# Kernel tuning notes

Measured on AMD Instinct MI355X. Metric: run time of the kernel, lower is better.

Reference implementation:

```python
import jax, jax.numpy as jnp
import numpy as np

N, E, ESM, H, OUT, L, NG = 20000, 640000, 1280, 128, 256, 3, 64
NV, EV = 4, 1  # node/edge vector channels
MSG_S, MSG_V = 2 * H + H, 2 * NV + EV   # 384, 9
UPD_S, UPD_V = 2 * H, 2 * NV            # 256, 8


def _safe_norm(v):
    # exact ||v|| with zero (not nan) gradient at v == 0
    n2 = jnp.sum(v * v, axis=-1)
    pos = n2 > 0
    return jnp.sqrt(jnp.where(pos, n2, 1.0)) * pos


def _normalize(x, eps=1e-12):
    n = _safe_norm(x)[..., None]
    return jnp.where(n > 0, x / jnp.maximum(n, eps), 0.0)


def _ln(x, g, b, eps=1e-5):
    m = x.mean(-1, keepdims=True)
    v = ((x - m) ** 2).mean(-1, keepdims=True)
    return (x - m) / jnp.sqrt(v + eps) * g + b


def _gvp(s, v, Wss, Wvs, Wsv, Wvv, g, b):
    # s: [M, Cs], v: [M, Cv, 3]
    vn = _safe_norm(v)                                        # [M, Cv]
    s_out = jax.nn.gelu(_ln(s @ Wss.T + vn @ Wvs.T, g, b), approximate=False)
    v_out = jnp.einsum('mic,oi->moc', v, Wvv)                 # [M, Cvo, 3]
    v_out = v_out * jax.nn.sigmoid(s @ Wsv.T)[:, :, None]     # gate from input s
    return s_out, v_out


def _compute_node_vectors(coords, cb):
    ca_cb = _normalize(cb - coords)
    ca_next = jnp.roll(coords, -1, axis=0)
    d = (ca_next - coords).at[-1].set(0.0)
    d = _normalize(d)
    normal = _normalize(jnp.cross(ca_cb, d))
    t = (ca_next - jnp.roll(coords, 1, axis=0)).at[0].set(0.0).at[-1].set(0.0)
    t = _normalize(t)
    return jnp.stack([ca_cb, d, normal, t], axis=1)           # [N, 4, 3]


def setup_inputs() -> dict:
    key = jax.random.key(0)
    ks = jax.random.split(key, 32)

    def w(k, shape):
        return (jax.random.normal(k, shape, jnp.float32) / np.sqrt(shape[-1])).astype(jnp.float32)

    inp = {
        'esm_features': jax.random.normal(ks[0], (N, ESM), jnp.float32),
        'geometric_features': jax.random.normal(ks[1], (N, 15), jnp.float32),
        'node_coords': jax.random.normal(ks[2], (N, 3), jnp.float32) * 10.0,
        'edge_index': jax.random.randint(ks[3], (2, E), 0, N, jnp.int32),
        'edge_attr': jax.random.normal(ks[4], (E, 16), jnp.float32),
        'batch_index': jnp.sort(jax.random.randint(ks[5], (N,), 0, NG, jnp.int32)),
        # projections
        'node_proj_W': w(ks[6], (H, ESM + 9)), 'node_proj_b': jnp.zeros((H,), jnp.float32),
        'edge_proj_W': w(ks[7], (H, 13)), 'edge_proj_b': jnp.zeros((H,), jnp.float32),
        # message GVP (stacked over L layers)
        'msg_Wss': w(ks[8], (L, H, MSG_S)), 'msg_Wvs': w(ks[9], (L, H, MSG_V)),
        'msg_Wsv': w(ks[10], (L, NV, MSG_S)), 'msg_Wvv': w(ks[11], (L, NV, MSG_V)),
        'msg_ln_g': jnp.ones((L, H), jnp.float32), 'msg_ln_b': jnp.zeros((L, H), jnp.float32),
        # update GVP
        'upd_Wss': w(ks[12], (L, H, UPD_S)), 'upd_Wvs': w(ks[13], (L, H, UPD_V)),
        'upd_Wsv': w(ks[14], (L, NV, UPD_S)), 'upd_Wvv': w(ks[15], (L, NV, UPD_V)),
        'upd_ln_g': jnp.ones((L, H), jnp.float32), 'upd_ln_b': jnp.zeros((L, H), jnp.float32),
        # heads
        'node_out_W': w(ks[16], (ESM, H)), 'node_out_b': jnp.zeros((ESM,), jnp.float32),
        'graph_out_W': w(ks[17], (OUT, H)), 'graph_out_b': jnp.zeros((OUT,), jnp.float32),
    }
    return inp


def reference(esm_features, geometric_features, node_coords, edge_index, edge_attr,
              batch_index, node_proj_W, node_proj_b, edge_proj_W, edge_proj_b,
              msg_Wss, msg_Wvs, msg_Wsv, msg_Wvv, msg_ln_g, msg_ln_b,
              upd_Wss, upd_Wvs, upd_Wsv, upd_Wvv, upd_ln_g, upd_ln_b,
              node_out_W, node_out_b, graph_out_W, graph_out_b):
    n = esm_features.shape[0]
    cb = geometric_features[:, 3:6]
    geo_scalar = geometric_features[:, 6:15]
    node_s = jnp.concatenate([esm_features, geo_scalar], -1) @ node_proj_W.T + node_proj_b
    node_v = _compute_node_vectors(node_coords, cb)
    edge_s = jnp.concatenate([edge_attr[:, 0:2], edge_attr[:, 5:]], -1) @ edge_proj_W.T + edge_proj_b
    edge_v = edge_attr[:, 2:5][:, None, :]                    # [E, 1, 3]
    src, dst = edge_index[0], edge_index[1]
    for l in range(msg_Wss.shape[0]):
        ms = jnp.concatenate([node_s[src], node_s[dst], edge_s], -1)   # [E, 3H]
        mv = jnp.concatenate([node_v[src], node_v[dst], edge_v], 1)    # [E, 9, 3]
        ms, mv = _gvp(ms, mv, msg_Wss[l], msg_Wvs[l], msg_Wsv[l], msg_Wvv[l],
                      msg_ln_g[l], msg_ln_b[l])
        ag_s = jnp.zeros((n, ms.shape[1]), ms.dtype).at[dst].add(ms)
        ag_v = jnp.zeros((n, mv.shape[1], 3), mv.dtype).at[dst].add(mv)
        us = jnp.concatenate([node_s, ag_s], -1)
        uv = jnp.concatenate([node_v, ag_v], 1)
        ns, nv = _gvp(us, uv, upd_Wss[l], upd_Wvs[l], upd_Wsv[l], upd_Wvv[l],
                      upd_ln_g[l], upd_ln_b[l])
        node_s = node_s + ns
        node_v = node_v + nv
    updated_nodes = node_s @ node_out_W.T + node_out_b
    gfeat = node_s @ graph_out_W.T + graph_out_b
    cnt = jax.ops.segment_sum(jnp.ones((n,), gfeat.dtype), batch_index, NG)
    graph_emb = jax.ops.segment_sum(gfeat, batch_index, NG) / jnp.maximum(cnt, 1.0)[:, None]
    return graph_emb, updated_nodes
```

## Files before the change

### kernel.cpp

```cpp
#include <hip/hip_runtime.h>
#include <math.h>

#define DEVI __device__ __forceinline__

namespace {

constexpr int NN = 20000;
constexpr int NE = 640000;

DEVI float gelu_f(float x){ return 0.5f*x*(1.0f+erff(x*0.70710678118654752440f)); }
DEVI float gelu_t(float x){
  float u = x*x;
  float z = x*(1.59576912f + 0.07135481f*u);
  return x / (1.f + __expf(-z));
}
DEVI float sigm(float x){ return 1.0f/(1.0f+expf(-x)); }
DEVI float sigm_f(float x){ return 1.0f/(1.0f+__expf(-x)); }

struct F3{ float x,y,z; };
DEVI F3 sub3(F3 a, F3 b){ return F3{a.x-b.x, a.y-b.y, a.z-b.z}; }
DEVI F3 cross3(F3 a, F3 b){ return F3{a.y*b.z-a.z*b.y, a.z*b.x-a.x*b.z, a.x*b.y-a.y*b.x}; }
DEVI F3 snorm3(F3 v){
  float n2 = v.x*v.x+v.y*v.y+v.z*v.z;
  if(n2 > 0.f){ float inv = 1.0f/sqrtf(n2); return F3{v.x*inv, v.y*inv, v.z*inv}; }
  return F3{0.f,0.f,0.f};
}

__global__ void k_tr(const float* __restrict__ src, float* __restrict__ dst,
                     int R, int C, int ld, int coff){
  int idx = blockIdx.x*256 + threadIdx.x;
  if(idx >= R*C) return;
  int r = idx / C, c = idx % C;
  dst[c*R + r] = src[r*ld + coff + c];
}

__global__ __launch_bounds__(256,4) void k_init(
                       const float* __restrict__ esm, const float* __restrict__ geo,
                       const float* __restrict__ Wt, const float* __restrict__ bias,
                       float* __restrict__ node_s){
  __shared__ float s_l[16][64];
  int t = threadIdx.x;
  int o = t&127, h = t>>7;
  int n0 = blockIdx.x*16;
  float acc[8];
#pragma unroll
  for(int i=0;i<8;i++) acc[i]=0.f;
  for(int k0=0;k0<1289;k0+=64){
    int kmax = (1289-k0 < 64) ? (1289-k0) : 64;
    for(int idx=t; idx<1024; idx+=256){
      int n = idx>>6, k = idx&63;
      float v = 0.f;
      int kk = k0+k;
      if(k < kmax){
        v = (kk<1280) ? esm[(size_t)(n0+n)*1280 + kk] : geo[(n0+n)*15 + 6 + (kk-1280)];
      }
      s_l[n][k] = v;
    }
    __syncthreads();
    int kq = kmax & ~3;
    for(int k=0;k<kq;k+=4){
      float w0 = Wt[(k0+k)*128+o];
      float w1 = Wt[(k0+k+1)*128+o];
      float w2 = Wt[(k0+k+2)*128+o];
      float w3 = Wt[(k0+k+3)*128+o];
#pragma unroll
      for(int n=0;n<8;n++){
        float4 s4 = *reinterpret_cast<const float4*>(&s_l[h*8+n][k]);
        acc[n] += s4.x*w0 + s4.y*w1 + s4.z*w2 + s4.w*w3;
      }
    }
    for(int k=kq;k<kmax;k++){
      float w = Wt[(k0+k)*128+o];
#pragma unroll
      for(int n=0;n<8;n++) acc[n] += s_l[h*8+n][k]*w;
    }
    __syncthreads();
  }
  float b = bias[o];
#pragma unroll
  for(int n=0;n<8;n++) node_s[(size_t)(n0+h*8+n)*128 + o] = acc[n] + b;
}

__global__ void k_nodevec(const float* __restrict__ coords, const float* __restrict__ geo,
                          float* __restrict__ node_v){
  int n = blockIdx.x*256 + threadIdx.x;
  if(n>=NN) return;
  F3 c  {coords[n*3], coords[n*3+1], coords[n*3+2]};
  F3 cb {geo[n*15+3], geo[n*15+4], geo[n*15+5]};
  F3 cacb = snorm3(sub3(cb, c));
  F3 d{0.f,0.f,0.f};
  if(n < NN-1){
    F3 nx {coords[(n+1)*3], coords[(n+1)*3+1], coords[(n+1)*3+2]};
    d = snorm3(sub3(nx, c));
  }
  F3 nor = snorm3(cross3(cacb, d));
  F3 tv{0.f,0.f,0.f};
  if(n>0 && n<NN-1){
    F3 nx {coords[(n+1)*3], coords[(n+1)*3+1], coords[(n+1)*3+2]};
    F3 pv {coords[(n-1)*3], coords[(n-1)*3+1], coords[(n-1)*3+2]};
    tv = snorm3(sub3(nx, pv));
  }
  float* p = node_v + n*12;
  p[0]=cacb.x; p[1]=cacb.y; p[2]=cacb.z;
  p[3]=d.x;    p[4]=d.y;    p[5]=d.z;
  p[6]=nor.x;  p[7]=nor.y;  p[8]=nor.z;
  p[9]=tv.x;   p[10]=tv.y;  p[11]=tv.z;
}

__global__ void k_hist(const int* __restrict__ eidx, int* __restrict__ counts){
  int e = blockIdx.x*256+threadIdx.x;
  if(e>=NE) return;
  atomicAdd(&counts[eidx[NE+e]], 1);
}
__global__ void k_cntg(const int* __restrict__ batch, int* __restrict__ cntg){
  int n = blockIdx.x*256+threadIdx.x;
  if(n>=NN) return;
  atomicAdd(&cntg[batch[n]], 1);
}
__global__ void k_scan1(const int* __restrict__ counts, int* __restrict__ bsums){
  __shared__ int red[256];
  int b=blockIdx.x, t=threadIdx.x;
  int base=b*512;
  int v=0;
  for(int i=t;i<512;i+=256){ int g=base+i; if(g<NN) v+=counts[g]; }
  red[t]=v; __syncthreads();
  for(int s=128;s;s>>=1){ if(t<s) red[t]+=red[t+s]; __syncthreads(); }
  if(t==0) bsums[b]=red[0];
}
__global__ void k_scan2(int* bsums){
  if(threadIdx.x==0 && blockIdx.x==0){
    int run=0;
    for(int i=0;i<40;i++){ int v=bsums[i]; bsums[i]=run; run+=v; }
  }
}
__global__ void k_scan3(const int* __restrict__ counts, const int* __restrict__ bsums,
                        int* __restrict__ offs){
  __shared__ int c_l[512];
  int b=blockIdx.x, t=threadIdx.x, base=b*512;
  for(int i=t;i<512;i+=256){ int g=base+i; c_l[i] = (g<NN)? counts[g]:0; }
  __syncthreads();
  if(t==0){
    int run=bsums[b];
    for(int i=0;i<512;i++){
      int g=base+i;
      if(g<NN) offs[g]=run;
      run += c_l[i];
    }
    if(b==39) offs[NN]=run;
  }
}
__global__ void k_fill(const int* __restrict__ eidx, int* __restrict__ cursor,
                       const float* __restrict__ eattr,
                       int* __restrict__ srcp, float* __restrict__ ea_s){
  int e = blockIdx.x*256+threadIdx.x;
  if(e>=NE) return;
  int d = eidx[NE+e];
  int s = eidx[e];
  int pos = atomicAdd(&cursor[d], 1);
  srcp[pos] = s;
  const float4* src4 = reinterpret_cast<const float4*>(eattr + (size_t)e*16);
  float4* dst4 = reinterpret_cast<float4*>(ea_s + (size_t)pos*16);
  dst4[0]=src4[0]; dst4[1]=src4[1]; dst4[2]=src4[2]; dst4[3]=src4[3];
}

__global__ __launch_bounds__(256,4) void k_pre(
                      const float* __restrict__ node_s, const float* __restrict__ node_v,
                      const float* __restrict__ Wt_ss, const float* __restrict__ Wt_vs,
                      const float* __restrict__ Wsv, const float* __restrict__ Wvv,
                      float* __restrict__ P_a, float* __restrict__ P_b,
                      float* __restrict__ G_a, float* __restrict__ G_b,
                      float* __restrict__ V_a, float* __restrict__ V_b){
  __shared__ float s_l[16][128];
  __shared__ float nv_l[16][4];
  __shared__ float uv[16][12];
  int t = threadIdx.x;
  int n0 = blockIdx.x*16;
  for(int idx=t; idx<2048; idx+=256){
    int n = idx>>7, k = idx&127;
    s_l[n][k] = node_s[(size_t)(n0+n)*128 + k];
  }
  if(t<192){ int n=t/12, k=t%12; uv[n][k] = node_v[(n0+n)*12+k]; }
  __syncthreads();
  if(t<64){
    int n=t>>2, j=t&3;
    float x=uv[n][j*3], y=uv[n][j*3+1], z=uv[n][j*3+2];
    float n2=x*x+y*y+z*z;
    nv_l[n][j] = n2>0.f ? sqrtf(n2) : 0.f;
  }
  if(t<192){
    int n=t/12, k=t%12, c=k/3, x=k-c*3;
    float va=0.f, vb=0.f;
#pragma unroll
    for(int j=0;j<4;j++){
      float vv = uv[n][j*3+x];
      va += Wvv[c*9+j]*vv;
      vb += Wvv[c*9+4+j]*vv;
    }
    V_a[(n0+n)*12+k]=va; V_b[(n0+n)*12+k]=vb;
  }
  if(t<128){
    int n=t>>3, c=(t>>1)&3, hh=t&1;
    const float* w = Wsv + c*384 + hh*128;
    float g=0.f;
    for(int k=0;k<128;k++) g += s_l[n][k]*w[k];
    (hh ? G_b : G_a)[(n0+n)*4+c] = g;
  }
  __syncthreads();
  int o = t&127, h = t>>7;
  float acc[16];
#pragma unroll
  for(int i=0;i<16;i++) acc[i]=0.f;
  const float* Wb = Wt_ss + h*128*128;
  for(int k=0;k<128;k++){
    float w = Wb[k*128+o];
#pragma unroll
    for(int n=0;n<16;n++) acc[n] += s_l[n][k]*w;
  }
  const float* Wv = Wt_vs + h*4*128;
#pragma unroll
  for(int j=0;j<4;j++){
    float w = Wv[j*128+o];
#pragma unroll
    for(int n=0;n<16;n++) acc[n] += nv_l[n][j]*w;
  }
  float* P = h ? P_b : P_a;
#pragma unroll
  for(int n=0;n<16;n++) P[(size_t)(n0+n)*128+o] = acc[n];
}

__global__ void k_econst(const float* __restrict__ Wss, const float* __restrict__ Wvs,
                         const float* __restrict__ Wsv, const float* __restrict__ Wvv,
                         const float* __restrict__ Wep, const float* __restrict__ epb,
                         float* __restrict__ ec){
  int t=threadIdx.x;
  for(int idx=t; idx<13*128; idx+=256){
    int j=idx>>7, o=idx&127;
    float s=0.f;
    for(int k=0;k<128;k++) s += Wss[o*384+256+k]*Wep[k*13+j];
    ec[j*128+o]=s;
  }
  for(int o=t;o<128;o+=256){
    float s=0.f;
    for(int k=0;k<128;k++) s += Wss[o*384+256+k]*epb[k];
    ec[1664+o]=s;
    ec[1792+o]=Wvs[o*9+8];
  }
  if(t<52){ int c=t/13,j=t%13; float s=0.f; for(int k=0;k<128;k++) s+=Wsv[c*384+256+k]*Wep[k*13+j]; ec[1920+t]=s; }
  if(t<4){ float s=0.f; for(int k=0;k<128;k++) s+=Wsv[t*384+256+k]*epb[k]; ec[1972+t]=s; ec[1976+t]=Wvv[t*9+8]; }
}

#define DECLST(P) int P##s=0; float4 P##A0{},P##A1{},P##A2{},P##A3{}; \
                  float P##pax=0.f,P##pay=0.f,P##ga=0.f,P##va=0.f;
#define LOADST(P, IDX) do{ int _p=(IDX); \
  P##s = srcp[_p]; \
  const float4* _ea = reinterpret_cast<const float4*>(ea_s + (size_t)_p*16); \
  P##A0=_ea[0]; P##A1=_ea[1]; P##A2=_ea[2]; P##A3=_ea[3]; \
  const float* _pa = P_a + (size_t)P##s*128; \
  P##pax=_pa[lane]; P##pay=_pa[64+lane]; \
  if(lane<12){ P##ga=G_a[(size_t)P##s*4+cv]; P##va=V_a[(size_t)P##s*12+lane]; } \
}while(0)
#define COMPUTE(P) do{ \
  float e0=P##A0.x,e1=P##A0.y,e2=P##A1.y,e3=P##A1.z,e4=P##A1.w, \
        e5=P##A2.x,e6=P##A2.y,e7=P##A2.z,e8=P##A2.w,e9=P##A3.x, \
        e10=P##A3.y,e11=P##A3.z,e12=P##A3.w; \
  float evx=P##A0.z, evy=P##A0.w, evz=P##A1.x; \
  float en2 = evx*evx+evy*evy+evz*evz; \
  float evn = en2>0.f ? sqrtf(en2) : 0.f; \
  float px = fmaf(evn,W8x, P##pax + Bx); \
  float py = fmaf(evn,W8y, P##pay + By); \
  px=fmaf(me2x[0],e0,px);   py=fmaf(me2y[0],e0,py); \
  px=fmaf(me2x[1],e1,px);   py=fmaf(me2y[1],e1,py); \
  px=fmaf(me2x[2],e2,px);   py=fmaf(me2y[2],e2,py); \
  px=fmaf(me2x[3],e3,px);   py=fmaf(me2y[3],e3,py); \
  px=fmaf(me2x[4],e4,px);   py=fmaf(me2y[4],e4,py); \
  px=fmaf(me2x[5],e5,px);   py=fmaf(me2y[5],e5,py); \
  px=fmaf(me2x[6],e6,px);   py=fmaf(me2y[6],e6,py); \
  px=fmaf(me2x[7],e7,px);   py=fmaf(me2y[7],e7,py); \
  px=fmaf(me2x[8],e8,px);   py=fmaf(me2y[8],e8,py); \
  px=fmaf(me2x[9],e9,px);   py=fmaf(me2y[9],e9,py); \
  px=fmaf(me2x[10],e10,px); py=fmaf(me2y[10],e10,py); \
  px=fmaf(me2x[11],e11,px); py=fmaf(me2y[11],e11,py); \
  px=fmaf(me2x[12],e12,px); py=fmaf(me2y[12],e12,py); \
  float sm = px+py; \
  float sq = px*px + py*py; \
  _Pragma("unroll") \
  for(int m=32;m;m>>=1){ sm += __shfl_xor(sm,m); sq += __shfl_xor(sq,m); } \
  float mean = sm*0.0078125f; \
  float var  = fmaf(sq,0.0078125f, -mean*mean); \
  float rstd = rsqrtf((var>0.f?var:0.f) + 1e-5f); \
  accx += gelu_t(fmaf((px-mean)*rstd, LGx, LBx)); \
  accy += gelu_t(fmaf((py-mean)*rstd, LGy, LBy)); \
  if(lane<12){ \
    const float* gcl = s_gcol + cv*13; \
    float g = P##ga + gbc; \
    g=fmaf(gcl[0],e0,g); g=fmaf(gcl[1],e1,g); g=fmaf(gcl[2],e2,g); \
    g=fmaf(gcl[3],e3,g); g=fmaf(gcl[4],e4,g); g=fmaf(gcl[5],e5,g); \
    g=fmaf(gcl[6],e6,g); g=fmaf(gcl[7],e7,g); g=fmaf(gcl[8],e8,g); \
    g=fmaf(gcl[9],e9,g); g=fmaf(gcl[10],e10,g); g=fmaf(gcl[11],e11,g); \
    g=fmaf(gcl[12],e12,g); \
    float gt = sigm_f(g); \
    float evc = (xv==0) ? evx : ((xv==1) ? evy : evz); \
    avk = fmaf(fmaf(wvc,evc, P##va + vbk), gt, avk); \
  } \
}while(0)

__global__ __launch_bounds__(256,4) void k_msg(
                      const float* __restrict__ P_a, const float* __restrict__ P_b,
                      const float* __restrict__ G_a, const float* __restrict__ G_b,
                      const float* __restrict__ V_a, const float* __restrict__ V_b,
                      const float* __restrict__ ea_s, const int* __restrict__ srcp,
                      const int* __restrict__ offs,
                      const float* __restrict__ ec,
                      const float* __restrict__ lng, const float* __restrict__ lnb,
                      float* __restrict__ ag_s, float* __restrict__ ag_v){
  __shared__ float s_gcol[52];
  int t = threadIdx.x;
  if(t<52) s_gcol[t]=ec[1920+t];
  int n = blockIdx.x*4 + (t>>6);
  int lane = t&63;
  float me2x[13], me2y[13];
#pragma unroll
  for(int j=0;j<13;j++){ me2x[j]=ec[j*128+lane]; me2y[j]=ec[j*128+64+lane]; }
  float Bx = ec[1664+lane]    + P_b[(size_t)n*128+lane];
  float By = ec[1664+64+lane] + P_b[(size_t)n*128+64+lane];
  float W8x = ec[1792+lane], W8y = ec[1792+64+lane];
  float LGx = lng[lane], LGy = lng[64+lane];
  float LBx = lnb[lane], LBy = lnb[64+lane];
  int cv = lane/3, xv = lane - cv*3;
  float vbk=0.f, gbc=0.f, wvc=0.f;
  if(lane<12){
    vbk = V_b[(size_t)n*12+lane];
    gbc = G_b[(size_t)n*4+cv] + ec[1972+cv];
    wvc = ec[1976+cv];
  }
  __syncthreads();
  float accx=0.f, accy=0.f, avk=0.f;
  int beg = offs[n], end = offs[n+1];
  DECLST(a_) DECLST(b_)
  int idx = beg;
  if(beg < end) LOADST(a_, beg);
  while(idx + 1 < end){
    LOADST(b_, idx+1);
    COMPUTE(a_);
    if(idx + 2 < end) LOADST(a_, idx+2);
    COMPUTE(b_);
    idx += 2;
  }
  if(idx < end) COMPUTE(a_);
  ag_s[(size_t)n*128+lane]    = accx;
  ag_s[(size_t)n*128+64+lane] = accy;
  if(lane<12) ag_v[(size_t)n*12+lane] = avk;
}

__global__ __launch_bounds__(256,4) void k_update(
                         float* __restrict__ node_s, float* __restrict__ node_v,
                         const float* __restrict__ ag_s, const float* __restrict__ ag_v,
                         const float* __restrict__ Wt_ss, const float* __restrict__ Wt_vs,
                         const float* __restrict__ Wsv, const float* __restrict__ Wvv,
                         const float* __restrict__ lng, const float* __restrict__ lnb){
  __shared__ float us[16][257];
  __shared__ float pre[16][129];
  __shared__ float uv[16][24];
  __shared__ float uvn[16][8];
  __shared__ float stats[16][2];
  __shared__ float gate_l[16][4];
  int t = threadIdx.x;
  int n0 = blockIdx.x*16;
  for(int idx=t; idx<2048; idx+=256){
    int n = idx>>7, k = idx&127;
    us[n][k]     = node_s[(size_t)(n0+n)*128+k];
    us[n][128+k] = ag_s[(size_t)(n0+n)*128+k];
  }
  for(int idx=t; idx<384; idx+=256){
    int n = idx/24, k = idx%24;
    uv[n][k] = (k<12) ? node_v[(n0+n)*12+k] : ag_v[(n0+n)*12 + (k-12)];
  }
  __syncthreads();
  if(t<128){
    int n=t>>3, j=t&7;
    float x=uv[n][j*3], y=uv[n][j*3+1], z=uv[n][j*3+2];
    float n2=x*x+y*y+z*z;
    uvn[n][j] = n2>0.f ? sqrtf(n2) : 0.f;
  }
  __syncthreads();
  int o = t&127, h = t>>7;
  float acc[8];
#pragma unroll
  for(int i=0;i<8;i++) acc[i]=0.f;
  for(int k=0;k<256;k++){
    float w = Wt_ss[k*128+o];
#pragma unroll
    for(int i=0;i<8;i++) acc[i] += us[h*8+i][k]*w;
  }
#pragma unroll
  for(int j=0;j<8;j++){
    float w = Wt_vs[j*128+o];
#pragma unroll
    for(int i=0;i<8;i++) acc[i] += uvn[h*8+i][j]*w;
  }
#pragma unroll
  for(int i=0;i<8;i++) pre[h*8+i][o] = acc[i];
  __syncthreads();
  {
    int n = t>>4, p = t&15;
    float s=0.f;
#pragma unroll
    for(int q=0;q<8;q++) s += pre[n][p*8+q];
#pragma unroll
    for(int m=8;m;m>>=1) s += __shfl_xor(s,m);
    float mean = s*(1.f/128.f);
    float v=0.f;
#pragma unroll
    for(int q=0;q<8;q++){ float d=pre[n][p*8+q]-mean; v += d*d; }
#pragma unroll
    for(int m=8;m;m>>=1) v += __shfl_xor(v,m);
    if(p==0){ stats[n][0]=mean; stats[n][1]=rsqrtf(v*(1.f/128.f)+1e-5f); }
  }
  __syncthreads();
  {
    float LG = lng[o], LB = lnb[o];
#pragma unroll
    for(int i=0;i<8;i++){
      int n = h*8+i;
      float hh = (pre[n][o]-stats[n][0])*stats[n][1]*LG + LB;
      node_s[(size_t)(n0+n)*128+o] += gelu_f(hh);
    }
  }
  {
    int n = t>>4, c = t&3, p = (t>>2)&3;
    float g=0.f;
    int kb = p*64;
    for(int k=0;k<64;k++) g += us[n][kb+k]*Wsv[c*256+kb+k];
    g += __shfl_xor(g,4);
    g += __shfl_xor(g,8);
    if(p==0) gate_l[n][c] = sigm(g);
  }
  __syncthreads();
  if(t<192){
    int n = t/12, k = t%12, c = k/3, x = k-c*3;
    float s=0.f;
#pragma unroll
    for(int j=0;j<8;j++) s += Wvv[c*8+j]*uv[n][j*3+x];
    node_v[(n0+n)*12+k] += s*gate_l[n][c];
  }
}

__global__ __launch_bounds__(256,4) void k_out(
                      const float* __restrict__ node_s, const float* __restrict__ Wt,
                      const float* __restrict__ bias, float* __restrict__ out){
  __shared__ float s_l[16][128];
  int t = threadIdx.x;
  int n0 = blockIdx.x*16;
  int o = blockIdx.y*256 + t;
  for(int idx=t; idx<2048; idx+=256){
    int n=idx>>7, k=idx&127;
    s_l[n][k] = node_s[(size_t)(n0+n)*128+k];
  }
  __syncthreads();
  float acc[16];
#pragma unroll
  for(int i=0;i<16;i++) acc[i]=0.f;
  for(int k=0;k<128;k++){
    float w = Wt[k*1280+o];
#pragma unroll
    for(int n=0;n<16;n++) acc[n] += s_l[n][k]*w;
  }
  float b = bias[o];
#pragma unroll
  for(int n=0;n<16;n++) out[16384 + (size_t)(n0+n)*1280 + o] = acc[n]+b;
}

__global__ __launch_bounds__(256,4) void k_gfeat(
                        const float* __restrict__ node_s, const float* __restrict__ Wt,
                        const int* __restrict__ batch, float* __restrict__ gacc){
  __shared__ float s_l[16][128];
  __shared__ int b_l[16];
  int t=threadIdx.x, n0=blockIdx.x*16;
  for(int idx=t; idx<2048; idx+=256){ int n=idx>>7,k=idx&127; s_l[n][k]=node_s[(size_t)(n0+n)*128+k]; }
  if(t<16) b_l[t]=batch[n0+t];
  __syncthreads();
  int o=t;
  float acc[16];
#pragma unroll
  for(int i=0;i<16;i++) acc[i]=0.f;
  for(int k=0;k<128;k++){
    float w=Wt[k*256+o];
#pragma unroll
    for(int n=0;n<16;n++) acc[n]+=s_l[n][k]*w;
  }
  float run=0.f; int cur=b_l[0];
#pragma unroll
  for(int n=0;n<16;n++){
    int g=b_l[n];
    if(g!=cur){ atomicAdd(&gacc[cur*256+o], run); run=0.f; cur=g; }
    run += acc[n];
  }
  atomicAdd(&gacc[cur*256+o], run);
}

__global__ void k_gfin(const float* __restrict__ gacc, const int* __restrict__ cntg,
                       const float* __restrict__ gob, float* __restrict__ out){
  int g=blockIdx.x, o=threadIdx.x;
  int c=cntg[g];
  out[g*256+o] = (c>0) ? (gacc[g*256+o]/(float)c + gob[o]) : 0.f;
}

}

extern "C" void kernel_launch(void* const* d_in, const int* in_sizes, int n_in,
                              void* d_out, int out_size, void* d_ws, size_t ws_size,
                              hipStream_t stream){
  (void)in_sizes; (void)n_in; (void)out_size;
  const float* esm   = (const float*)d_in[0];
  const float* geo   = (const float*)d_in[1];
  const float* coords= (const float*)d_in[2];
  const int*   eidx  = (const int*)d_in[3];
  const float* eattr = (const float*)d_in[4];
  const int*   batch = (const int*)d_in[5];
  const float* npW   = (const float*)d_in[6];
  const float* npb   = (const float*)d_in[7];
  const float* epW   = (const float*)d_in[8];
  const float* epb   = (const float*)d_in[9];
  const float* mWss  = (const float*)d_in[10];
  const float* mWvs  = (const float*)d_in[11];
  const float* mWsv  = (const float*)d_in[12];
  const float* mWvv  = (const float*)d_in[13];
  const float* mlg   = (const float*)d_in[14];
  const float* mlb   = (const float*)d_in[15];
  const float* uWss  = (const float*)d_in[16];
  const float* uWvs  = (const float*)d_in[17];
  const float* uWsv  = (const float*)d_in[18];
  const float* uWvv  = (const float*)d_in[19];
  const float* ulg   = (const float*)d_in[20];
  const float* ulb   = (const float*)d_in[21];
  const float* noW   = (const float*)d_in[22];
  const float* nob   = (const float*)d_in[23];
  const float* goW   = (const float*)d_in[24];
  const float* gob   = (const float*)d_in[25];
  float* out = (float*)d_out;

  char* base = (char*)d_ws;
  size_t off = 0;
  auto ALLOC = [&](size_t bytes)->char*{
    char* p = base + off;
    off = (off + bytes + 255) & ~(size_t)255;
    return p;
  };
  float* node_s = (float*)ALLOC((size_t)NN*128*4);
  float* P_a    = (float*)ALLOC((size_t)NN*128*4);
  float* P_b    = (float*)ALLOC((size_t)NN*128*4);
  float* ag_s   = (float*)ALLOC((size_t)NN*128*4);
  float* node_v = (float*)ALLOC((size_t)NN*12*4);
  float* ag_v   = (float*)ALLOC((size_t)NN*12*4);
  float* V_a    = (float*)ALLOC((size_t)NN*12*4);
  float* V_b    = (float*)ALLOC((size_t)NN*12*4);
  float* G_a    = (float*)ALLOC((size_t)NN*4*4);
  float* G_b    = (float*)ALLOC((size_t)NN*4*4);
  float* Wt_np  = (float*)ALLOC((size_t)1289*128*4);
  float* Wt_no  = (float*)ALLOC((size_t)128*1280*4);
  float* Wt_go  = (float*)ALLOC((size_t)128*256*4);
  float* Wt_mss = (float*)ALLOC((size_t)3*256*128*4);
  float* Wt_mvs = (float*)ALLOC((size_t)3*9*128*4);
  float* Wt_uss = (float*)ALLOC((size_t)3*256*128*4);
  float* Wt_uvs = (float*)ALLOC((size_t)3*8*128*4);
  float* econ   = (float*)ALLOC((size_t)3*2048*4);
  float* gacc   = (float*)ALLOC((size_t)64*256*4);
  int* counts = (int*)ALLOC((size_t)NN*4);
  int* offs   = (int*)ALLOC((size_t)(NN+1)*4);
  int* cursor = (int*)ALLOC((size_t)NN*4);
  int* bsums  = (int*)ALLOC((size_t)64*4);
  int* cntg   = (int*)ALLOC((size_t)64*4);
  int* srcp   = (int*)ALLOC((size_t)NE*4);
  float* ea_s = (float*)ALLOC((size_t)NE*16*4);
  if(off > ws_size) return;

  hipMemsetAsync(counts, 0, (size_t)NN*4, stream);
  hipMemsetAsync(cntg,   0, 64*4, stream);
  hipMemsetAsync(gacc,   0, (size_t)64*256*4, stream);

  k_tr<<<645,256,0,stream>>>(npW, Wt_np, 128, 1289, 1289, 0);
  k_tr<<<640,256,0,stream>>>(noW, Wt_no, 1280, 128, 128, 0);
  k_tr<<<128,256,0,stream>>>(goW, Wt_go, 256, 128, 128, 0);
  for(int l=0;l<3;l++){
    k_tr<<<128,256,0,stream>>>(mWss + (size_t)l*128*384, Wt_mss + (size_t)l*256*128, 128, 256, 384, 0);
    k_tr<<<5,  256,0,stream>>>(mWvs + (size_t)l*128*9,   Wt_mvs + (size_t)l*9*128,   128, 9,   9,   0);
    k_tr<<<128,256,0,stream>>>(uWss + (size_t)l*128*256, Wt_uss + (size_t)l*256*128, 128, 256, 256, 0);
    k_tr<<<4,  256,0,stream>>>(uWvs + (size_t)l*128*8,   Wt_uvs + (size_t)l*8*128,   128, 8,   8,   0);
  }
  k_init<<<1250,256,0,stream>>>(esm, geo, Wt_np, npb, node_s);
  k_nodevec<<<79,256,0,stream>>>(coords, geo, node_v);
  k_hist<<<2500,256,0,stream>>>(eidx, counts);
  k_scan1<<<40,256,0,stream>>>(counts, bsums);
  k_scan2<<<1,64,0,stream>>>(bsums);
  k_scan3<<<40,256,0,stream>>>(counts, bsums, offs);
  hipMemcpyAsync(cursor, offs, (size_t)NN*4, hipMemcpyDeviceToDevice, stream);
  k_fill<<<2500,256,0,stream>>>(eidx, cursor, eattr, srcp, ea_s);
  k_cntg<<<79,256,0,stream>>>(batch, cntg);

  for(int l=0;l<3;l++){
    k_pre<<<1250,256,0,stream>>>(node_s, node_v,
                                 Wt_mss + (size_t)l*256*128, Wt_mvs + (size_t)l*9*128,
                                 mWsv + (size_t)l*4*384, mWvv + (size_t)l*4*9,
                                 P_a, P_b, G_a, G_b, V_a, V_b);
    k_econst<<<1,256,0,stream>>>(mWss + (size_t)l*128*384, mWvs + (size_t)l*128*9,
                                 mWsv + (size_t)l*4*384, mWvv + (size_t)l*4*9,
                                 epW, epb, econ + (size_t)l*2048);
    k_msg<<<5000,256,0,stream>>>(P_a, P_b, G_a, G_b, V_a, V_b, ea_s, srcp, offs,
                                 econ + (size_t)l*2048, mlg + (size_t)l*128, mlb + (size_t)l*128,
                                 ag_s, ag_v);
    k_update<<<1250,256,0,stream>>>(node_s, node_v, ag_s, ag_v,
                                    Wt_uss + (size_t)l*256*128, Wt_uvs + (size_t)l*8*128,
                                    uWsv + (size_t)l*4*256, uWvv + (size_t)l*4*8,
                                    ulg + (size_t)l*128, ulb + (size_t)l*128);
  }
  k_out<<<dim3(1250,5),256,0,stream>>>(node_s, Wt_no, nob, out);
  k_gfeat<<<1250,256,0,stream>>>(node_s, Wt_go, batch, gacc);
  k_gfin<<<64,256,0,stream>>>(gacc, cntg, gob, out);
}
```

Baseline: 1.809 ms.

## Merge small setup kernels and launches to cut launch overhead

Fifteen weight-transpose launches are merged into one k_prep kernel, and the counts/cntg memsets are folded into k_nodevec. The histogram kernels are merged, scan2/scan3 and the cursor memcpy become one kernel, the per-layer econst launches become a single 3-block launch, and the output and graph-feature GEMMs share one grid. k_msg now holds the gate coefficients in registers instead of shared memory, which removes a block barrier, and its launch bound drops to 2 blocks per SM. The aim is to cut launch count and per-kernel fixed overhead, at the cost of more register pressure in k_msg and a serial prefix loop in each scan block.

```diff
diff --git a/kernel.cpp b/kernel.cpp
--- a/kernel.cpp
+++ b/kernel.cpp
@@ -26,12 +26,30 @@
   return F3{0.f,0.f,0.f};
 }
 
-__global__ void k_tr(const float* __restrict__ src, float* __restrict__ dst,
-                     int R, int C, int ld, int coff){
-  int idx = blockIdx.x*256 + threadIdx.x;
-  if(idx >= R*C) return;
-  int r = idx / C, c = idx % C;
-  dst[c*R + r] = src[r*ld + coff + c];
+__global__ void k_prep(const float* __restrict__ npW, const float* __restrict__ noW,
+                       const float* __restrict__ goW,
+                       const float* __restrict__ mWss, const float* __restrict__ mWvs,
+                       const float* __restrict__ uWss, const float* __restrict__ uWvs,
+                       float* __restrict__ Wt_np, float* __restrict__ Wt_no,
+                       float* __restrict__ Wt_go,
+                       float* __restrict__ Wt_mss, float* __restrict__ Wt_mvs,
+                       float* __restrict__ Wt_uss, float* __restrict__ Wt_uvs){
+  int b = blockIdx.x, t = threadIdx.x;
+  const float* src; float* dst; int R,C,ld,base,elems;
+  if(b<645){ src=npW; dst=Wt_np; R=128;C=1289;ld=1289; base=0; elems=164992; }
+  else if(b<1285){ src=noW; dst=Wt_no; R=1280;C=128;ld=128; base=645; elems=163840; }
+  else if(b<1413){ src=goW; dst=Wt_go; R=256;C=128;ld=128; base=1285; elems=32768; }
+  else {
+    int bb=b-1413; int l=bb/265; int r=bb-l*265;
+    if(r<128){ src=mWss+(size_t)l*128*384; dst=Wt_mss+(size_t)l*256*128; R=128;C=256;ld=384; base=1413+l*265; elems=32768; }
+    else if(r<133){ src=mWvs+(size_t)l*128*9; dst=Wt_mvs+(size_t)l*9*128; R=128;C=9;ld=9; base=1413+l*265+128; elems=1152; }
+    else if(r<261){ src=uWss+(size_t)l*128*256; dst=Wt_uss+(size_t)l*256*128; R=128;C=256;ld=256; base=1413+l*265+133; elems=32768; }
+    else { src=uWvs+(size_t)l*128*8; dst=Wt_uvs+(size_t)l*8*128; R=128;C=8;ld=8; base=1413+l*265+261; elems=1024; }
+  }
+  int idx=(b-base)*256+t;
+  if(idx>=elems) return;
+  int r=idx/C, c=idx%C;
+  dst[c*R+r] = src[r*ld+c];
 }
 
 __global__ __launch_bounds__(256,4) void k_init(
@@ -82,9 +100,12 @@
 }
 
 __global__ void k_nodevec(const float* __restrict__ coords, const float* __restrict__ geo,
-                          float* __restrict__ node_v){
+                          float* __restrict__ node_v,
+                          int* __restrict__ counts, int* __restrict__ cntg){
   int n = blockIdx.x*256 + threadIdx.x;
+  if(n<64) cntg[n]=0;
   if(n>=NN) return;
+  counts[n]=0;
   F3 c  {coords[n*3], coords[n*3+1], coords[n*3+2]};
   F3 cb {geo[n*15+3], geo[n*15+4], geo[n*15+5]};
   F3 cacb = snorm3(sub3(cb, c));
@@ -107,15 +128,11 @@
   p[9]=tv.x;   p[10]=tv.y;  p[11]=tv.z;
 }
 
-__global__ void k_hist(const int* __restrict__ eidx, int* __restrict__ counts){
-  int e = blockIdx.x*256+threadIdx.x;
-  if(e>=NE) return;
-  atomicAdd(&counts[eidx[NE+e]], 1);
-}
-__global__ void k_cntg(const int* __restrict__ batch, int* __restrict__ cntg){
-  int n = blockIdx.x*256+threadIdx.x;
-  if(n>=NN) return;
-  atomicAdd(&cntg[batch[n]], 1);
+__global__ void k_hist(const int* __restrict__ eidx, const int* __restrict__ batch,
+                       int* __restrict__ counts, int* __restrict__ cntg){
+  int i = blockIdx.x*256+threadIdx.x;
+  if(i<NE) atomicAdd(&counts[eidx[NE+i]], 1);
+  if(i<NN) atomicAdd(&cntg[batch[i]], 1);
 }
 __global__ void k_scan1(const int* __restrict__ counts, int* __restrict__ bsums){
   __shared__ int red[256];
@@ -127,23 +144,18 @@
   for(int s=128;s;s>>=1){ if(t<s) red[t]+=red[t+s]; __syncthreads(); }
   if(t==0) bsums[b]=red[0];
 }
-__global__ void k_scan2(int* bsums){
-  if(threadIdx.x==0 && blockIdx.x==0){
-    int run=0;
-    for(int i=0;i<40;i++){ int v=bsums[i]; bsums[i]=run; run+=v; }
-  }
-}
-__global__ void k_scan3(const int* __restrict__ counts, const int* __restrict__ bsums,
-                        int* __restrict__ offs){
+__global__ void k_scan23(const int* __restrict__ counts, const int* __restrict__ bsums,
+                         int* __restrict__ offs, int* __restrict__ cursor){
   __shared__ int c_l[512];
   int b=blockIdx.x, t=threadIdx.x, base=b*512;
   for(int i=t;i<512;i+=256){ int g=base+i; c_l[i] = (g<NN)? counts[g]:0; }
   __syncthreads();
   if(t==0){
-    int run=bsums[b];
+    int run=0;
+    for(int i=0;i<b;i++) run += bsums[i];
     for(int i=0;i<512;i++){
       int g=base+i;
-      if(g<NN) offs[g]=run;
+      if(g<NN){ offs[g]=run; cursor[g]=run; }
       run += c_l[i];
     }
     if(b==39) offs[NN]=run;
@@ -228,10 +240,16 @@
   for(int n=0;n<16;n++) P[(size_t)(n0+n)*128+o] = acc[n];
 }
 
-__global__ void k_econst(const float* __restrict__ Wss, const float* __restrict__ Wvs,
-                         const float* __restrict__ Wsv, const float* __restrict__ Wvv,
-                         const float* __restrict__ Wep, const float* __restrict__ epb,
-                         float* __restrict__ ec){
+__global__ void k_econst3(const float* __restrict__ mWss, const float* __restrict__ mWvs,
+                          const float* __restrict__ mWsv, const float* __restrict__ mWvv,
+                          const float* __restrict__ Wep, const float* __restrict__ epb,
+                          float* __restrict__ econ){
+  int l = blockIdx.x;
+  const float* Wss = mWss + (size_t)l*128*384;
+  const float* Wvs = mWvs + (size_t)l*128*9;
+  const float* Wsv = mWsv + (size_t)l*4*384;
+  const float* Wvv = mWvv + (size_t)l*4*9;
+  float* ec = econ + (size_t)l*2048;
   int t=threadIdx.x;
   for(int idx=t; idx<13*128; idx+=256){
     int j=idx>>7, o=idx&127;
@@ -291,20 +309,19 @@
   accx += gelu_t(fmaf((px-mean)*rstd, LGx, LBx)); \
   accy += gelu_t(fmaf((py-mean)*rstd, LGy, LBy)); \
   if(lane<12){ \
-    const float* gcl = s_gcol + cv*13; \
     float g = P##ga + gbc; \
-    g=fmaf(gcl[0],e0,g); g=fmaf(gcl[1],e1,g); g=fmaf(gcl[2],e2,g); \
-    g=fmaf(gcl[3],e3,g); g=fmaf(gcl[4],e4,g); g=fmaf(gcl[5],e5,g); \
-    g=fmaf(gcl[6],e6,g); g=fmaf(gcl[7],e7,g); g=fmaf(gcl[8],e8,g); \
-    g=fmaf(gcl[9],e9,g); g=fmaf(gcl[10],e10,g); g=fmaf(gcl[11],e11,g); \
-    g=fmaf(gcl[12],e12,g); \
+    g=fmaf(grc[0],e0,g); g=fmaf(grc[1],e1,g); g=fmaf(grc[2],e2,g); \
+    g=fmaf(grc[3],e3,g); g=fmaf(grc[4],e4,g); g=fmaf(grc[5],e5,g); \
+    g=fmaf(grc[6],e6,g); g=fmaf(grc[7],e7,g); g=fmaf(grc[8],e8,g); \
+    g=fmaf(grc[9],e9,g); g=fmaf(grc[10],e10,g); g=fmaf(grc[11],e11,g); \
+    g=fmaf(grc[12],e12,g); \
     float gt = sigm_f(g); \
     float evc = (xv==0) ? evx : ((xv==1) ? evy : evz); \
     avk = fmaf(fmaf(wvc,evc, P##va + vbk), gt, avk); \
   } \
 }while(0)
 
-__global__ __launch_bounds__(256,4) void k_msg(
+__global__ __launch_bounds__(256,2) void k_msg(
                       const float* __restrict__ P_a, const float* __restrict__ P_b,
                       const float* __restrict__ G_a, const float* __restrict__ G_b,
                       const float* __restrict__ V_a, const float* __restrict__ V_b,
@@ -313,9 +330,7 @@
                       const float* __restrict__ ec,
                       const float* __restrict__ lng, const float* __restrict__ lnb,
                       float* __restrict__ ag_s, float* __restrict__ ag_v){
-  __shared__ float s_gcol[52];
   int t = threadIdx.x;
-  if(t<52) s_gcol[t]=ec[1920+t];
   int n = blockIdx.x*4 + (t>>6);
   int lane = t&63;
   float me2x[13], me2y[13];
@@ -327,13 +342,16 @@
   float LGx = lng[lane], LGy = lng[64+lane];
   float LBx = lnb[lane], LBy = lnb[64+lane];
   int cv = lane/3, xv = lane - cv*3;
+  int cvg = (lane<12) ? cv : 0;
+  float grc[13];
+#pragma unroll
+  for(int j=0;j<13;j++) grc[j] = ec[1920 + cvg*13 + j];
   float vbk=0.f, gbc=0.f, wvc=0.f;
   if(lane<12){
     vbk = V_b[(size_t)n*12+lane];
     gbc = G_b[(size_t)n*4+cv] + ec[1972+cv];
     wvc = ec[1976+cv];
   }
-  __syncthreads();
   float accx=0.f, accy=0.f, avk=0.f;
   int beg = offs[n], end = offs[n+1];
   DECLST(a_) DECLST(b_)
@@ -445,57 +463,54 @@
   }
 }
 
-__global__ __launch_bounds__(256,4) void k_out(
-                      const float* __restrict__ node_s, const float* __restrict__ Wt,
-                      const float* __restrict__ bias, float* __restrict__ out){
+__global__ __launch_bounds__(256,4) void k_outg(
+                      const float* __restrict__ node_s, const float* __restrict__ Wt_no,
+                      const float* __restrict__ nob, const float* __restrict__ Wt_go,
+                      const int* __restrict__ batch, float* __restrict__ gacc,
+                      float* __restrict__ out){
   __shared__ float s_l[16][128];
+  __shared__ int b_l[16];
   int t = threadIdx.x;
   int n0 = blockIdx.x*16;
-  int o = blockIdx.y*256 + t;
+  int y = blockIdx.y;
   for(int idx=t; idx<2048; idx+=256){
     int n=idx>>7, k=idx&127;
     s_l[n][k] = node_s[(size_t)(n0+n)*128+k];
   }
-  __syncthreads();
-  float acc[16];
-#pragma unroll
-  for(int i=0;i<16;i++) acc[i]=0.f;
-  for(int k=0;k<128;k++){
-    float w = Wt[k*1280+o];
-#pragma unroll
-    for(int n=0;n<16;n++) acc[n] += s_l[n][k]*w;
-  }
-  float b = bias[o];
-#pragma unroll
-  for(int n=0;n<16;n++) out[16384 + (size_t)(n0+n)*1280 + o] = acc[n]+b;
-}
-
-__global__ __launch_bounds__(256,4) void k_gfeat(
-                        const float* __restrict__ node_s, const float* __restrict__ Wt,
-                        const int* __restrict__ batch, float* __restrict__ gacc){
-  __shared__ float s_l[16][128];
-  __shared__ int b_l[16];
-  int t=threadIdx.x, n0=blockIdx.x*16;
-  for(int idx=t; idx<2048; idx+=256){ int n=idx>>7,k=idx&127; s_l[n][k]=node_s[(size_t)(n0+n)*128+k]; }
-  if(t<16) b_l[t]=batch[n0+t];
-  __syncthreads();
-  int o=t;
-  float acc[16];
-#pragma unroll
-  for(int i=0;i<16;i++) acc[i]=0.f;
-  for(int k=0;k<128;k++){
-    float w=Wt[k*256+o];
-#pragma unroll
-    for(int n=0;n<16;n++) acc[n]+=s_l[n][k]*w;
-  }
-  float run=0.f; int cur=b_l[0];
-#pragma unroll
-  for(int n=0;n<16;n++){
-    int g=b_l[n];
-    if(g!=cur){ atomicAdd(&gacc[cur*256+o], run); run=0.f; cur=g; }
-    run += acc[n];
-  }
-  atomicAdd(&gacc[cur*256+o], run);
+  if(y==5 && t<16) b_l[t]=batch[n0+t];
+  __syncthreads();
+  if(y<5){
+    int o = y*256 + t;
+    float acc[16];
+#pragma unroll
+    for(int i=0;i<16;i++) acc[i]=0.f;
+    for(int k=0;k<128;k++){
+      float w = Wt_no[k*1280+o];
+#pragma unroll
+      for(int n=0;n<16;n++) acc[n] += s_l[n][k]*w;
+    }
+    float b = nob[o];
+#pragma unroll
+    for(int n=0;n<16;n++) out[16384 + (size_t)(n0+n)*1280 + o] = acc[n]+b;
+  } else {
+    int o=t;
+    float acc[16];
+#pragma unroll
+    for(int i=0;i<16;i++) acc[i]=0.f;
+    for(int k=0;k<128;k++){
+      float w=Wt_go[k*256+o];
+#pragma unroll
+      for(int n=0;n<16;n++) acc[n]+=s_l[n][k]*w;
+    }
+    float run=0.f; int cur=b_l[0];
+#pragma unroll
+    for(int n=0;n<16;n++){
+      int g=b_l[n];
+      if(g!=cur){ atomicAdd(&gacc[cur*256+o], run); run=0.f; cur=g; }
+      run += acc[n];
+    }
+    atomicAdd(&gacc[cur*256+o], run);
+  }
 }
 
 __global__ void k_gfin(const float* __restrict__ gacc, const int* __restrict__ cntg,
@@ -574,37 +589,23 @@
   float* ea_s = (float*)ALLOC((size_t)NE*16*4);
   if(off > ws_size) return;
 
-  hipMemsetAsync(counts, 0, (size_t)NN*4, stream);
-  hipMemsetAsync(cntg,   0, 64*4, stream);
-  hipMemsetAsync(gacc,   0, (size_t)64*256*4, stream);
-
-  k_tr<<<645,256,0,stream>>>(npW, Wt_np, 128, 1289, 1289, 0);
-  k_tr<<<640,256,0,stream>>>(noW, Wt_no, 1280, 128, 128, 0);
-  k_tr<<<128,256,0,stream>>>(goW, Wt_go, 256, 128, 128, 0);
-  for(int l=0;l<3;l++){
-    k_tr<<<128,256,0,stream>>>(mWss + (size_t)l*128*384, Wt_mss + (size_t)l*256*128, 128, 256, 384, 0);
-    k_tr<<<5,  256,0,stream>>>(mWvs + (size_t)l*128*9,   Wt_mvs + (size_t)l*9*128,   128, 9,   9,   0);
-    k_tr<<<128,256,0,stream>>>(uWss + (size_t)l*128*256, Wt_uss + (size_t)l*256*128, 128, 256, 256, 0);
-    k_tr<<<4,  256,0,stream>>>(uWvs + (size_t)l*128*8,   Wt_uvs + (size_t)l*8*128,   128, 8,   8,   0);
-  }
+  hipMemsetAsync(gacc, 0, (size_t)64*256*4, stream);
+
+  k_prep<<<2208,256,0,stream>>>(npW, noW, goW, mWss, mWvs, uWss, uWvs,
+                                Wt_np, Wt_no, Wt_go, Wt_mss, Wt_mvs, Wt_uss, Wt_uvs);
   k_init<<<1250,256,0,stream>>>(esm, geo, Wt_np, npb, node_s);
-  k_nodevec<<<79,256,0,stream>>>(coords, geo, node_v);
-  k_hist<<<2500,256,0,stream>>>(eidx, counts);
+  k_nodevec<<<79,256,0,stream>>>(coords, geo, node_v, counts, cntg);
+  k_hist<<<2500,256,0,stream>>>(eidx, batch, counts, cntg);
   k_scan1<<<40,256,0,stream>>>(counts, bsums);
-  k_scan2<<<1,64,0,stream>>>(bsums);
-  k_scan3<<<40,256,0,stream>>>(counts, bsums, offs);
-  hipMemcpyAsync(cursor, offs, (size_t)NN*4, hipMemcpyDeviceToDevice, stream);
+  k_scan23<<<40,256,0,stream>>>(counts, bsums, offs, cursor);
   k_fill<<<2500,256,0,stream>>>(eidx, cursor, eattr, srcp, ea_s);
-  k_cntg<<<79,256,0,stream>>>(batch, cntg);
+  k_econst3<<<3,256,0,stream>>>(mWss, mWvs, mWsv, mWvv, epW, epb, econ);
 
   for(int l=0;l<3;l++){
     k_pre<<<1250,256,0,stream>>>(node_s, node_v,
                                  Wt_mss + (size_t)l*256*128, Wt_mvs + (size_t)l*9*128,
                                  mWsv + (size_t)l*4*384, mWvv + (size_t)l*4*9,
                                  P_a, P_b, G_a, G_b, V_a, V_b);
-    k_econst<<<1,256,0,stream>>>(mWss + (size_t)l*128*384, mWvs + (size_t)l*128*9,
-                                 mWsv + (size_t)l*4*384, mWvv + (size_t)l*4*9,
-                                 epW, epb, econ + (size_t)l*2048);
     k_msg<<<5000,256,0,stream>>>(P_a, P_b, G_a, G_b, V_a, V_b, ea_s, srcp, offs,
                                  econ + (size_t)l*2048, mlg + (size_t)l*128, mlb + (size_t)l*128,
                                  ag_s, ag_v);
@@ -613,7 +614,6 @@
                                     uWsv + (size_t)l*4*256, uWvv + (size_t)l*4*8,
                                     ulg + (size_t)l*128, ulb + (size_t)l*128);
   }
-  k_out<<<dim3(1250,5),256,0,stream>>>(node_s, Wt_no, nob, out);
-  k_gfeat<<<1250,256,0,stream>>>(node_s, Wt_go, batch, gacc);
+  k_outg<<<dim3(1250,6),256,0,stream>>>(node_s, Wt_no, nob, Wt_go, batch, gacc, out);
   k_gfin<<<64,256,0,stream>>>(gacc, cntg, gob, out);
 }
```

New measurement: 1.741 ms. 1.04x faster.
